# Performance work log

Hardware: AMD Instinct MI355X
Metric: run time of the kernel (lower is better)

Reference implementation:

```python
import jax, jax.numpy as jnp
import numpy as np


def setup_inputs() -> dict:
    key = jax.random.key(0)
    k1, k2 = jax.random.split(key)
    B, C, H, W = 4, 64, 256, 256
    x = jax.random.normal(k1, (B, C, H, W), dtype=jnp.float32)
    perspective = jax.random.uniform(k2, (B, 1, H, W), dtype=jnp.float32)
    alpha = jnp.ones((1,), dtype=jnp.float32) * 3.0   # sigma scale
    beta = jnp.ones((1,), dtype=jnp.float32)          # sigmoid slope
    gamma = jnp.zeros((1,), dtype=jnp.float32)        # sigmoid shift
    return {"x": x, "perspective": perspective, "alpha": alpha,
            "beta": beta, "gamma": gamma, "kernel_size": 7}


def reference(x, perspective, alpha, beta, gamma, kernel_size):
    K = int(kernel_size)
    pad = K // 2
    B, C, H, W = x.shape
    # AdaptiveSigmoid sigma map, clamped like the torch module
    sigma = jnp.maximum(alpha * jax.nn.sigmoid(beta * perspective + gamma), 1e-4)  # [B,1,H,W]
    inv2s2 = 1.0 / (2.0 * sigma * sigma)                                           # [B,1,H,W]
    # squared distance of each kernel tap from center (static)
    offs = np.arange(K) - pad
    d2 = (offs[:, None] ** 2 + offs[None, :] ** 2).reshape(-1).astype(np.float32)  # [K*K]
    # per-pixel, per-tap Gaussian weights, normalized over taps
    w = jnp.exp(-d2[:, None, None, None, None] * inv2s2[None])  # [K*K,B,1,H,W]
    w = w / jnp.sum(w, axis=0)
    xp = jnp.pad(x, ((0, 0), (0, 0), (pad, pad), (pad, pad)))
    out = jnp.zeros_like(x)
    k = 0
    for i in range(K):            # fixed small K*K loop (49 taps), jit-friendly
        for j in range(K):
            out = out + w[k] * xp[:, :, i:i + H, j:j + W]
            k += 1
    return out
```

## Files before the change

### kernel.cpp

```cpp
#include <hip/hip_runtime.h>

#define NB 4
#define NC 64
#define NH 256
#define NW 256
#define TH 64

__device__ __attribute__((aligned(64))) float zbuf[16];

__global__ __launch_bounds__(256, 2)
void adaptive_gauss7(const float* __restrict__ x,
                     const float* __restrict__ persp,
                     const float* __restrict__ alpha_p,
                     const float* __restrict__ beta_p,
                     const float* __restrict__ gamma_p,
                     float* __restrict__ out)
{
    const int tid  = threadIdx.x;
    const int lane = tid & 63;
    const int wv   = tid >> 6;
    const int c    = blockIdx.x;
    const int h0   = blockIdx.y * TH;
    const int b    = blockIdx.z;
    const int colbase = lane * 4;
    const int rg      = h0 + wv * 16;

    const float alpha = alpha_p[0];
    const float beta  = beta_p[0];
    const float gamma = gamma_p[0];

    const float* xc = x     + (size_t)(b * NC + c) * NH * NW;
    const float* pp = persp + (size_t)b * NH * NW;
    float*     outp = out   + (size_t)(b * NC + c) * NH * NW;

    float win[7][12];

    auto loadrow = [&](float dst[12], int gr) {
        const bool rv = (unsigned)gr < NH;
        const float* p  = xc + (size_t)gr * NW + colbase;
        const float* p0 = (rv && lane != 0)  ? (p - 4) : zbuf;
        const float* p1 =  rv                ?  p      : zbuf;
        const float* p2 = (rv && lane != 63) ? (p + 4) : zbuf;
        const float4 a0 = *(const float4*)p0;
        const float4 a1 = *(const float4*)p1;
        const float4 a2 = *(const float4*)p2;
        dst[0] = a0.x; dst[1] = a0.y; dst[2]  = a0.z; dst[3]  = a0.w;
        dst[4] = a1.x; dst[5] = a1.y; dst[6]  = a1.z; dst[7]  = a1.w;
        dst[8] = a2.x; dst[9] = a2.y; dst[10] = a2.z; dst[11] = a2.w;
    };

    #pragma unroll
    for (int r = 0; r < 7; ++r)
        loadrow(win[r], rg - 3 + r);

    float4 pvn = *(const float4*)(pp + (size_t)rg * NW + colbase);

    #pragma unroll
    for (int o = 0; o < 16; ++o) {
        float nxt[12];
        if (o < 15)
            loadrow(nxt, rg + o + 4);

        const float4 pv = pvn;
        if (o < 15)
            pvn = *(const float4*)(pp + (size_t)(rg + o + 1) * NW + colbase);

        const float pva[4] = {pv.x, pv.y, pv.z, pv.w};
        float res[4];
        #pragma unroll
        for (int k = 0; k < 4; ++k) {
            const float z  = fmaf(beta, pva[k], gamma);
            const float sg = __builtin_amdgcn_rcpf(1.0f + __expf(-z));
            const float sigma = fmaxf(alpha * sg, 1e-4f);
            const float t  = 0.5f * __builtin_amdgcn_rcpf(sigma * sigma);
            const float g  = __expf(-t);
            const float g2 = g * g;
            const float p4 = g2 * g2;
            const float p9 = p4 * p4 * g;
            const float S  = fmaf(2.0f, (g + p4) + p9, 1.0f);
            const float inv  = __builtin_amdgcn_rcpf(S);
            const float inv2 = inv * inv;

            float rs[7];
            #pragma unroll
            for (int j = 0; j < 7; ++j) {
                const int s = (o + j) % 7;
                rs[j] = fmaf(p9, win[s][k+1] + win[s][k+7],
                        fmaf(p4, win[s][k+2] + win[s][k+6],
                        fmaf(g,  win[s][k+3] + win[s][k+5],
                                 win[s][k+4])));
            }
            const float acc = fmaf(p9, rs[0] + rs[6],
                              fmaf(p4, rs[1] + rs[5],
                              fmaf(g,  rs[2] + rs[4],
                                       rs[3])));
            res[k] = acc * inv2;
        }
        *(float4*)(outp + (size_t)(rg + o) * NW + colbase) =
            make_float4(res[0], res[1], res[2], res[3]);

        if (o < 15) {
            const int s = o % 7;
            #pragma unroll
            for (int q = 0; q < 12; ++q)
                win[s][q] = nxt[q];
        }
    }
}

extern "C" void kernel_launch(void* const* d_in, const int* in_sizes, int n_in,
                              void* d_out, int out_size, void* d_ws, size_t ws_size,
                              hipStream_t stream) {
    const float* x     = (const float*)d_in[0];
    const float* persp = (const float*)d_in[1];
    const float* alpha = (const float*)d_in[2];
    const float* beta  = (const float*)d_in[3];
    const float* gamma = (const float*)d_in[4];
    float* outp        = (float*)d_out;
    dim3 grid(NC, NH / TH, NB);
    adaptive_gauss7<<<grid, dim3(256), 0, stream>>>(x, persp, alpha, beta, gamma, outp);
}
```

Before: 142.7 us.

## Precompute per-pixel gaussian weights and stage input tiles in LDS

Adds a prep kernel that computes the per-pixel Gaussian base weight and normalization once per batch into workspace, instead of recomputing the sigmoid/exp chain for every channel. The main kernel now stages a 22-row padded tile in shared memory with zero halos and reads the 7x7 neighborhood from LDS rather than issuing three overlapping global loads per row. Tiles shrink from 64 to 16 rows, with higher occupancy hints. The trade-offs are an extra kernel launch, extra workspace traffic (two floats per pixel read by every channel), and a larger fraction of halo rows reloaded per tile.

Result: slower. 228.3 us (+60.0%).

```diff
diff --git a/kernel.cpp b/kernel.cpp
--- a/kernel.cpp
+++ b/kernel.cpp
@@ -4,18 +4,51 @@
 #define NC 64
 #define NH 256
 #define NW 256
-#define TH 64
+#define TH 16
+#define SROWS (TH + 6)
+#define LROW 264
 
-__device__ __attribute__((aligned(64))) float zbuf[16];
+__global__ __launch_bounds__(256)
+void wprep(const float* __restrict__ persp,
+           const float* __restrict__ alpha_p,
+           const float* __restrict__ beta_p,
+           const float* __restrict__ gamma_p,
+           float* __restrict__ ws)
+{
+    const float alpha = alpha_p[0];
+    const float beta  = beta_p[0];
+    const float gamma = gamma_p[0];
+    const int i = (blockIdx.x * 256 + threadIdx.x) * 4;
+    const float4 p = *(const float4*)(persp + i);
+    const float pa[4] = {p.x, p.y, p.z, p.w};
+    float g[4], inv2[4];
+    #pragma unroll
+    for (int k = 0; k < 4; ++k) {
+        const float z  = fmaf(beta, pa[k], gamma);
+        const float sg = __builtin_amdgcn_rcpf(1.0f + __expf(-z));
+        const float sigma = fmaxf(alpha * sg, 1e-4f);
+        const float t  = 0.5f * __builtin_amdgcn_rcpf(sigma * sigma);
+        const float gg = __expf(-t);
+        const float g2 = gg * gg;
+        const float p4 = g2 * g2;
+        const float p9 = p4 * p4 * gg;
+        const float S  = fmaf(2.0f, (gg + p4) + p9, 1.0f);
+        const float inv = __builtin_amdgcn_rcpf(S);
+        g[k] = gg;
+        inv2[k] = inv * inv;
+    }
+    float* wp = ws + (size_t)i * 2;
+    *(float4*)(wp)     = make_float4(g[0], inv2[0], g[1], inv2[1]);
+    *(float4*)(wp + 4) = make_float4(g[2], inv2[2], g[3], inv2[3]);
+}
 
-__global__ __launch_bounds__(256, 2)
+__global__ __launch_bounds__(256, 4)
 void adaptive_gauss7(const float* __restrict__ x,
-                     const float* __restrict__ persp,
-                     const float* __restrict__ alpha_p,
-                     const float* __restrict__ beta_p,
-                     const float* __restrict__ gamma_p,
+                     const float* __restrict__ wsr,
                      float* __restrict__ out)
 {
+    __shared__ float lds[SROWS * LROW];
+
     const int tid  = threadIdx.x;
     const int lane = tid & 63;
     const int wv   = tid >> 6;
@@ -23,88 +56,82 @@
     const int h0   = blockIdx.y * TH;
     const int b    = blockIdx.z;
     const int colbase = lane * 4;
-    const int rg      = h0 + wv * 16;
+    const int rg      = h0 + wv * 4;
 
-    const float alpha = alpha_p[0];
-    const float beta  = beta_p[0];
-    const float gamma = gamma_p[0];
+    const float* xc   = x   + (size_t)(b * NC + c) * NH * NW;
+    float*       outp = out + (size_t)(b * NC + c) * NH * NW;
+    const float* wrow = wsr + (size_t)b * NH * NW * 2;
 
-    const float* xc = x     + (size_t)(b * NC + c) * NH * NW;
-    const float* pp = persp + (size_t)b * NH * NW;
-    float*     outp = out   + (size_t)(b * NC + c) * NH * NW;
+    if (tid < SROWS)
+        *(float4*)&lds[tid * LROW] = make_float4(0.f, 0.f, 0.f, 0.f);
+    else if (tid < 2 * SROWS)
+        *(float4*)&lds[(tid - SROWS) * LROW + 260] = make_float4(0.f, 0.f, 0.f, 0.f);
 
-    float win[7][12];
+    for (int r = wv; r < SROWS; r += 4) {
+        const int gr = h0 - 3 + r;
+        float4 v = make_float4(0.f, 0.f, 0.f, 0.f);
+        if ((unsigned)gr < NH)
+            v = *(const float4*)(xc + (size_t)gr * NW + colbase);
+        *(float4*)&lds[r * LROW + 4 + colbase] = v;
+    }
+    __syncthreads();
 
-    auto loadrow = [&](float dst[12], int gr) {
-        const bool rv = (unsigned)gr < NH;
-        const float* p  = xc + (size_t)gr * NW + colbase;
-        const float* p0 = (rv && lane != 0)  ? (p - 4) : zbuf;
-        const float* p1 =  rv                ?  p      : zbuf;
-        const float* p2 = (rv && lane != 63) ? (p + 4) : zbuf;
-        const float4 a0 = *(const float4*)p0;
-        const float4 a1 = *(const float4*)p1;
-        const float4 a2 = *(const float4*)p2;
-        dst[0] = a0.x; dst[1] = a0.y; dst[2]  = a0.z; dst[3]  = a0.w;
-        dst[4] = a1.x; dst[5] = a1.y; dst[6]  = a1.z; dst[7]  = a1.w;
-        dst[8] = a2.x; dst[9] = a2.y; dst[10] = a2.z; dst[11] = a2.w;
-    };
+    const float* wp0 = wrow + ((size_t)rg * NW + colbase) * 2;
+    float4 wa = *(const float4*)(wp0);
+    float4 wb = *(const float4*)(wp0 + 4);
 
     #pragma unroll
-    for (int r = 0; r < 7; ++r)
-        loadrow(win[r], rg - 3 + r);
+    for (int o = 0; o < 4; ++o) {
+        float4 na, nb;
+        if (o < 3) {
+            const float* wp = wrow + ((size_t)(rg + o + 1) * NW + colbase) * 2;
+            na = *(const float4*)(wp);
+            nb = *(const float4*)(wp + 4);
+        }
 
-    float4 pvn = *(const float4*)(pp + (size_t)rg * NW + colbase);
+        const float gk[4] = {wa.x, wa.z, wb.x, wb.z};
+        const float iv[4] = {wa.y, wa.w, wb.y, wb.w};
+        float g[4], p4[4], p9[4];
+        #pragma unroll
+        for (int k = 0; k < 4; ++k) {
+            g[k] = gk[k];
+            const float g2 = g[k] * g[k];
+            p4[k] = g2 * g2;
+            p9[k] = p4[k] * p4[k] * g[k];
+        }
 
-    #pragma unroll
-    for (int o = 0; o < 16; ++o) {
-        float nxt[12];
-        if (o < 15)
-            loadrow(nxt, rg + o + 4);
+        float rs[7][4];
+        #pragma unroll
+        for (int j = 0; j < 7; ++j) {
+            const float* rp = &lds[(wv * 4 + o + j) * LROW + colbase];
+            const float4 r0 = *(const float4*)(rp);
+            const float4 r1 = *(const float4*)(rp + 4);
+            const float4 r2 = *(const float4*)(rp + 8);
+            const float w[12] = {r0.x, r0.y, r0.z, r0.w,
+                                 r1.x, r1.y, r1.z, r1.w,
+                                 r2.x, r2.y, r2.z, r2.w};
+            #pragma unroll
+            for (int k = 0; k < 4; ++k) {
+                rs[j][k] = fmaf(p9[k], w[k + 1] + w[k + 7],
+                           fmaf(p4[k], w[k + 2] + w[k + 6],
+                           fmaf(g[k],  w[k + 3] + w[k + 5],
+                                       w[k + 4])));
+            }
+        }
 
-        const float4 pv = pvn;
-        if (o < 15)
-            pvn = *(const float4*)(pp + (size_t)(rg + o + 1) * NW + colbase);
-
-        const float pva[4] = {pv.x, pv.y, pv.z, pv.w};
         float res[4];
         #pragma unroll
         for (int k = 0; k < 4; ++k) {
-            const float z  = fmaf(beta, pva[k], gamma);
-            const float sg = __builtin_amdgcn_rcpf(1.0f + __expf(-z));
-            const float sigma = fmaxf(alpha * sg, 1e-4f);
-            const float t  = 0.5f * __builtin_amdgcn_rcpf(sigma * sigma);
-            const float g  = __expf(-t);
-            const float g2 = g * g;
-            const float p4 = g2 * g2;
-            const float p9 = p4 * p4 * g;
-            const float S  = fmaf(2.0f, (g + p4) + p9, 1.0f);
-            const float inv  = __builtin_amdgcn_rcpf(S);
-            const float inv2 = inv * inv;
-
-            float rs[7];
-            #pragma unroll
-            for (int j = 0; j < 7; ++j) {
-                const int s = (o + j) % 7;
-                rs[j] = fmaf(p9, win[s][k+1] + win[s][k+7],
-                        fmaf(p4, win[s][k+2] + win[s][k+6],
-                        fmaf(g,  win[s][k+3] + win[s][k+5],
-                                 win[s][k+4])));
-            }
-            const float acc = fmaf(p9, rs[0] + rs[6],
-                              fmaf(p4, rs[1] + rs[5],
-                              fmaf(g,  rs[2] + rs[4],
-                                       rs[3])));
-            res[k] = acc * inv2;
+            const float acc = fmaf(p9[k], rs[0][k] + rs[6][k],
+                              fmaf(p4[k], rs[1][k] + rs[5][k],
+                              fmaf(g[k],  rs[2][k] + rs[4][k],
+                                          rs[3][k])));
+            res[k] = acc * iv[k];
         }
         *(float4*)(outp + (size_t)(rg + o) * NW + colbase) =
             make_float4(res[0], res[1], res[2], res[3]);
 
-        if (o < 15) {
-            const int s = o % 7;
-            #pragma unroll
-            for (int q = 0; q < 12; ++q)
-                win[s][q] = nxt[q];
-        }
+        if (o < 3) { wa = na; wb = nb; }
     }
 }
 
@@ -117,6 +144,8 @@
     const float* beta  = (const float*)d_in[3];
     const float* gamma = (const float*)d_in[4];
     float* outp        = (float*)d_out;
-    dim3 grid(NC, NH / TH, NB);
-    adaptive_gauss7<<<grid, dim3(256), 0, stream>>>(x, persp, alpha, beta, gamma, outp);
+    float* ws          = (float*)d_ws;
+
+    wprep<<<dim3((NB * NH * NW) / 1024), dim3(256), 0, stream>>>(persp, alpha, beta, gamma, ws);
+    adaptive_gauss7<<<dim3(NC, NH / TH, NB), dim3(256), 0, stream>>>(x, ws, outp);
 }
```
